# Kernel optimization log

Measured on AMD Instinct MI355X. Metric: run time of the kernel, lower is better.

The kernel has to match this reference:

```python
import jax, jax.numpy as jnp
import numpy as np
import math

IMG = 256      # image H = W (img_shape)
N_ANG = 360    # projection views over [0, pi)
N_DET = 256    # radial detector bins
N_SAMP = 256   # samples along each ray
VOX = 2.0      # voxel size / detector bin width in mm (isotropic)
FWHM = 4.0     # gaussian_PSF FWHM in mm


def _gauss_kernel(sigma):
    radius = max(1, int(math.ceil(3.0 * sigma)))
    t = np.arange(-radius, radius + 1, dtype=np.float64)
    k = np.exp(-0.5 * (t / sigma) ** 2)
    return (k / k.sum()).astype(np.float32), radius


def _blur_axis(x, sigma, axis):
    """1-D Gaussian blur with reflect padding along `axis` (static small kernel)."""
    k, r = _gauss_kernel(sigma)
    x = jnp.moveaxis(x, axis, -1)
    L = x.shape[-1]
    pad = [(0, 0)] * (x.ndim - 1) + [(r, r)]
    xp = jnp.pad(x, pad, mode='reflect')
    out = sum(float(k[i]) * xp[..., i:i + L] for i in range(2 * r + 1))
    return jnp.moveaxis(out, -1, axis)


def _blur2d(x, sigma):
    return _blur_axis(_blur_axis(x, sigma, -1), sigma, -2)


def _geometry():
    """Static parallel-beam ray-sampling geometry (bilinear taps, in pixel units)."""
    theta = np.pi * np.arange(N_ANG) / N_ANG
    r = (np.arange(N_DET) - (N_DET - 1) / 2.0) * VOX   # detector offsets [mm]
    s = (np.arange(N_SAMP) - (N_SAMP - 1) / 2.0) * VOX  # depth along ray [mm]
    cos = np.cos(theta)[:, None, None]
    sin = np.sin(theta)[:, None, None]
    x = r[None, :, None] * cos - s[None, None, :] * sin  # (A, D, S) mm
    y = r[None, :, None] * sin + s[None, None, :] * cos
    ix = x / VOX + (IMG - 1) / 2.0
    iy = y / VOX + (IMG - 1) / 2.0
    valid = ((ix >= 0) & (ix <= IMG - 1) & (iy >= 0) & (iy <= IMG - 1)).astype(np.float32)
    j0 = np.clip(np.floor(ix).astype(np.int32), 0, IMG - 2)
    i0 = np.clip(np.floor(iy).astype(np.int32), 0, IMG - 2)
    fx = (ix - j0).astype(np.float32)
    fy = (iy - i0).astype(np.float32)
    return i0, j0, fy, fx, valid

_GEO = tuple(jnp.asarray(a) for a in _geometry())


def _project(img):
    """Parallel-view 2D ray projection: img (B,H,W) -> sinogram (B, N_DET, N_ANG)."""
    i0, j0, fy, fx, valid = _GEO
    v00 = img[:, i0, j0]
    v01 = img[:, i0, j0 + 1]
    v10 = img[:, i0 + 1, j0]
    v11 = img[:, i0 + 1, j0 + 1]
    vals = ((1 - fy) * (1 - fx) * v00 + (1 - fy) * fx * v01
            + fy * (1 - fx) * v10 + fy * fx * v11) * valid
    sino = vals.sum(-1) * VOX          # (B, N_ANG, N_DET), line integral in mm
    return jnp.transpose(sino, (0, 2, 1))  # (B, N_DET, N_ANG)


def setup_inputs() -> dict:
    key = jax.random.key(0)
    k1, k2 = jax.random.split(key)
    image = jax.random.uniform(k1, (2, 1, IMG, IMG), dtype=jnp.float32)
    attenuation_map = jax.random.uniform(k2, (2, 1, IMG, IMG), dtype=jnp.float32)
    return {"image": image, "attenuation_map": attenuation_map}


def reference(image, attenuation_map):
    sqrt_log2 = math.sqrt(math.log(2.0))
    sigma_img = (FWHM / (4.0 * sqrt_log2)) / VOX
    # emission PSF blur (reflect) then project
    img_b = _blur2d(image, sigma_img)
    sino = _project(img_b[:, 0])[:, None]          # (B,1,N_DET,N_ANG)
    # attenuation: wider PSF blur, 0.01 scale, project, exponential scaling
    sigma_att = (FWHM / (2.0 * sqrt_log2)) / VOX
    att_b = _blur2d(attenuation_map, sigma_att) * 0.01
    att_sino = _project(att_b[:, 0])[:, None]
    sino = sino * jnp.exp(-att_sino * VOX)
    # column-wise (detector axis) sinogram PSF
    sino = _blur_axis(sino, sigma_img, -2)
    return sino
```

## Files before the change

kernel.cpp:

```cpp
#include <hip/hip_runtime.h>
#include <math.h>

#define IMG 256
#define N_ANG 360
#define N_DET 256

#define NH_BLOCKS 181
#define NV_BLOCKS (179 * 32)
#define EPS 1e-3f

struct W9 { float w[9]; };
struct AngTab { double c, sn; float cf, snf; float pad0, pad1; };

typedef _Float16 h2 __attribute__((ext_vector_type(2)));

#if __has_builtin(__builtin_amdgcn_fdot2)
__device__ __forceinline__ float fdot2(h2 a, h2 b, float c) {
    return __builtin_amdgcn_fdot2(a, b, c, false);
}
#else
__device__ __forceinline__ float fdot2(h2 a, h2 b, float c) {
    return c + (float)a[0] * (float)b[0] + (float)a[1] * (float)b[1];
}
#endif

__device__ __forceinline__ h2 as_h2(unsigned u) { return __builtin_bit_cast(h2, u); }
__device__ __forceinline__ unsigned pack2(float a, float b) {
    h2 v = { (_Float16)a, (_Float16)b };
    return __builtin_bit_cast(unsigned, v);
}

__device__ __forceinline__ int refl(int i, int L) {
    if (i < 0) i = -i;
    if (i >= L) i = 2 * (L - 1) - i;
    return i;
}

__global__ void blurpix_k(const float* __restrict__ img, const float* __restrict__ att,
                          uint4* __restrict__ pix2, AngTab* __restrict__ tab,
                          W9 wi, W9 wa) {
    int x = threadIdx.x, y = blockIdx.x;
    int gid = y * IMG + x;
    if (gid < N_ANG) {
        double th = M_PI * (double)gid / 360.0;
        double c = cos(th), sn = sin(th);
        AngTab tb;
        tb.c = c; tb.sn = sn; tb.cf = (float)c; tb.snf = (float)sn;
        tb.pad0 = 0.f; tb.pad1 = 0.f;
        tab[gid] = tb;
    }
    float v[4];
    #pragma unroll
    for (int m = 0; m < 4; ++m) {
        const float* src = ((m & 1) ? att : img) + (m >> 1) * IMG * IMG;
        const float* w = (m & 1) ? wa.w : wi.w;
        const int r = (m & 1) ? 4 : 2;
        float acc = 0.f;
        for (int dy = -r; dy <= r; ++dy) {
            const float* rowp = src + refl(y + dy, IMG) * IMG;
            float ra = 0.f;
            for (int dx = -r; dx <= r; ++dx) ra += w[dx + r] * rowp[refl(x + dx, IMG)];
            acc += w[dy + r] * ra;
        }
        v[m] = acc * ((m & 1) ? 0.01f : 1.0f);
    }
    __shared__ float4 row[IMG];
    row[x] = make_float4(v[0], v[1], v[2], v[3]);
    __syncthreads();
    float4 rn = row[min(x + 1, IMG - 1)];
    uint4 o;
    o.x = pack2(v[0], rn.x);
    o.y = pack2(v[1], rn.y);
    o.z = pack2(v[2], rn.z);
    o.w = pack2(v[3], rn.w);
    pix2[gid] = o;
}

template <typename P>
__device__ __forceinline__ int lastTrue(P p) {
    if (!p(0)) return -1;
    if (p(255)) return 255;
    int lo = 0, hi = 255;
    while (lo < hi) { int m = (lo + hi + 1) >> 1; if (p(m)) lo = m; else hi = m - 1; }
    return lo;
}
template <typename P>
__device__ __forceinline__ int firstTrue(P p) {
    if (!p(255)) return 256;
    if (p(0)) return 0;
    int lo = 0, hi = 255;
    while (lo < hi) { int m = (lo + hi) >> 1; if (p(m)) hi = m; else lo = m + 1; }
    return lo;
}

__device__ __forceinline__ void tap_acc(const uint4* __restrict__ pix2,
                                        int i0, int j0,
                                        float w00, float w01, float w10, float w11,
                                        float4& acc) {
    h2 wt = { (_Float16)w00, (_Float16)w01 };
    h2 wb = { (_Float16)w10, (_Float16)w11 };
    const uint4* p0 = pix2 + (i0 << 8) + j0;
    uint4 T = p0[0];
    uint4 B = p0[IMG];
    acc.x = fdot2(as_h2(T.x), wt, acc.x);
    acc.x = fdot2(as_h2(B.x), wb, acc.x);
    acc.y = fdot2(as_h2(T.y), wt, acc.y);
    acc.y = fdot2(as_h2(B.y), wb, acc.y);
    acc.z = fdot2(as_h2(T.z), wt, acc.z);
    acc.z = fdot2(as_h2(B.z), wb, acc.z);
    acc.w = fdot2(as_h2(T.w), wt, acc.w);
    acc.w = fdot2(as_h2(B.w), wb, acc.w);
}

__global__ __launch_bounds__(512) void proj_k(const uint4* __restrict__ pix2,
                                              const AngTab* __restrict__ tab,
                                              float4* __restrict__ part4,
                                              float* __restrict__ out, W9 wblur) {
    int t = threadIdx.x;
    int bx = blockIdx.x;

    if (bx < NH_BLOCKS) {
        int d = t & 255, kc = t >> 8;
        int a = (bx <= 90) ? bx : bx + 179;
        AngTab tb = tab[a];
        double rr = (double)(2 * d - 255);
        double rc = __dmul_rn(rr, tb.c), rs = __dmul_rn(rr, tb.sn);

        auto evIx = [&](int k) -> double {
            double ss = (double)(2 * k - 255);
            return __dadd_rn(__dmul_rn(__dsub_rn(rc, __dmul_rn(ss, tb.sn)), 0.5), 127.5);
        };
        auto evIy = [&](int k) -> double {
            double ss = (double)(2 * k - 255);
            return __dadd_rn(__dmul_rn(__dadd_rn(rs, __dmul_rn(ss, tb.c)), 0.5), 127.5);
        };
        int khiA = lastTrue([&](int k) { return evIx(k) >= 0.0; });
        int kloA = firstTrue([&](int k) { return evIx(k) <= 255.0; });
        int kloB, khiB;
        if (tb.c > 0.0) {
            kloB = firstTrue([&](int k) { return evIy(k) >= 0.0; });
            khiB = lastTrue([&](int k) { return evIy(k) <= 255.0; });
        } else {
            khiB = lastTrue([&](int k) { return evIy(k) >= 0.0; });
            kloB = firstTrue([&](int k) { return evIy(k) <= 255.0; });
        }
        int lo = max(kloA, kloB), hi = min(khiA, khiB);
        lo = max(lo, kc * 128); hi = min(hi, kc * 128 + 127);
        if (lo > hi) { lo = 0; hi = -1; }

        int jl = (hi >= lo) ? lo : 0x7fffffff;
        int jh = (hi >= lo) ? hi : (-0x7fffffff - 1);
        #pragma unroll
        for (int off = 32; off; off >>= 1) {
            jl = min(jl, __shfl_xor(jl, off));
            jh = max(jh, __shfl_xor(jh, off));
        }

        float x0f = (float)evIx(128);
        float y0f = (float)evIy(128);
        float dxf = -tb.snf, dyf = tb.cf;

        float4 acc = make_float4(0.f, 0.f, 0.f, 0.f);
        for (int kb = jl; kb <= jh; kb += 4) {
            #pragma unroll
            for (int u = 0; u < 4; ++u) {
                int k = kb + u;
                float kf = (float)(k - 128);
                float ixf = fmaf(kf, dxf, x0f);
                float iyf = fmaf(kf, dyf, y0f);
                float m = (k >= lo && k <= hi) ? 2.0f : 0.0f;
                int j0 = (int)ixf; j0 = min(max(j0, 0), 254);
                int i0 = (int)iyf; i0 = min(max(i0, 0), 254);
                float fx = ixf - (float)j0;
                float fy = iyf - (float)i0;
                float gxm = (1.f - fx) * m, fxm = fx * m;
                float gy = 1.f - fy;
                tap_acc(pix2, i0, j0, gy * gxm, gy * fxm, fy * gxm, fy * fxm, acc);
            }
        }

        __shared__ float4 red[512];
        __shared__ float vb[2][N_DET];
        red[t] = acc;
        __syncthreads();
        if (t < 256) {
            float4 u = red[t], v = red[t + 256];
            float si0 = u.x + v.x, sa0 = u.y + v.y;
            float si1 = u.z + v.z, sa1 = u.w + v.w;
            vb[0][t] = si0 * expf(-sa0 * 2.0f);
            vb[1][t] = si1 * expf(-sa1 * 2.0f);
        }
        __syncthreads();
        if (t < 256) {
            float a0 = 0.f, a1 = 0.f;
            #pragma unroll
            for (int i = -2; i <= 2; ++i) {
                int dd = refl(t + i, N_DET);
                a0 += wblur.w[i + 2] * vb[0][dd];
                a1 += wblur.w[i + 2] * vb[1][dd];
            }
            out[t * N_ANG + a] = a0;
            out[(N_DET + t) * N_ANG + a] = a1;
        }
    } else {
        int idx = bx - NH_BLOCKS;
        int a = 91 + (idx >> 5);
        int dgrp = idx & 31;
        int lane = t & 63, w = t >> 6;
        int d = dgrp * 8 + w;
        AngTab tb = tab[a];
        float cf = tb.cf, snf = tb.snf;
        float df = (float)d - 127.5f;
        float hx = fmaf(df, cf, 127.5f);
        float hy = fmaf(df, snf, 127.5f);

        float4 acc = make_float4(0.f, 0.f, 0.f, 0.f);
        #pragma unroll
        for (int j = 0; j < 4; ++j) {
            int k = j * 64 + lane;
            float kf = (float)k - 127.5f;
            float ixf = fmaf(-kf, snf, hx);
            float iyf = fmaf(kf, cf, hy);
            float vmin = fminf(fminf(ixf, 255.0f - ixf), fminf(iyf, 255.0f - iyf));
            if (!__any(vmin > -EPS)) continue;
            float m = (vmin >= EPS) ? 2.0f : 0.0f;
            if (fabsf(vmin) < EPS) {
                double ss = (double)(2 * k - 255);
                double rr = (double)(2 * d - 255);
                double rc = __dmul_rn(rr, tb.c), rs = __dmul_rn(rr, tb.sn);
                double ixd = __dadd_rn(__dmul_rn(__dsub_rn(rc, __dmul_rn(ss, tb.sn)), 0.5), 127.5);
                double iyd = __dadd_rn(__dmul_rn(__dadd_rn(rs, __dmul_rn(ss, tb.c)), 0.5), 127.5);
                bool v = (ixd >= 0.0) && (ixd <= 255.0) && (iyd >= 0.0) && (iyd <= 255.0);
                m = v ? 2.0f : 0.0f;
            }
            int j0 = (int)ixf; j0 = min(max(j0, 0), 254);
            int i0 = (int)iyf; i0 = min(max(i0, 0), 254);
            float fx = ixf - (float)j0;
            float fy = iyf - (float)i0;
            float gxm = (1.f - fx) * m, fxm = fx * m;
            float gy = 1.f - fy;
            tap_acc(pix2, i0, j0, gy * gxm, gy * fxm, fy * gxm, fy * fxm, acc);
        }

        #pragma unroll
        for (int off = 32; off; off >>= 1) {
            acc.x += __shfl_xor(acc.x, off);
            acc.y += __shfl_xor(acc.y, off);
            acc.z += __shfl_xor(acc.z, off);
            acc.w += __shfl_xor(acc.w, off);
        }
        if (lane == 0) part4[a * N_DET + d] = acc;
    }
}

__global__ __launch_bounds__(256) void finish_v_k(const float4* __restrict__ part4,
                                                  float* __restrict__ out, W9 wt) {
    int d = threadIdx.x;
    int b = blockIdx.x / 179;
    int a = 91 + (blockIdx.x % 179);
    float4 s = part4[a * N_DET + d];
    float si = b ? s.z : s.x;
    float sa = b ? s.w : s.y;
    __shared__ float vb[N_DET];
    vb[d] = si * expf(-sa * 2.0f);
    __syncthreads();
    float acc = 0.f;
    #pragma unroll
    for (int i = -2; i <= 2; ++i) acc += wt.w[i + 2] * vb[refl(d + i, N_DET)];
    out[(b * N_DET + d) * N_ANG + a] = acc;
}

static void gauss_w(W9* wt, double sigma, int r) {
    double tmp[9];
    double s = 0.0;
    for (int i = -r; i <= r; ++i) {
        double v = exp(-0.5 * ((double)i / sigma) * ((double)i / sigma));
        tmp[i + r] = v;
        s += v;
    }
    for (int i = 0; i < 9; ++i) wt->w[i] = 0.f;
    for (int i = 0; i < 2 * r + 1; ++i) wt->w[i] = (float)(tmp[i] / s);
}

extern "C" void kernel_launch(void* const* d_in, const int* in_sizes, int n_in,
                              void* d_out, int out_size, void* d_ws, size_t ws_size,
                              hipStream_t stream) {
    const float* img = (const float*)d_in[0];
    const float* att = (const float*)d_in[1];
    float* out = (float*)d_out;

    char* ws = (char*)d_ws;
    AngTab* tab = (AngTab*)ws;
    uint4* pix2 = (uint4*)(ws + 16384);
    float4* part4 = (float4*)(ws + 16384 + (1 << 20));

    double sqrt_log2 = sqrt(log(2.0));
    double sigma_img = 4.0 / (4.0 * sqrt_log2) / 2.0;
    double sigma_att = 4.0 / (2.0 * sqrt_log2) / 2.0;
    W9 wimg, watt;
    gauss_w(&wimg, sigma_img, 2);
    gauss_w(&watt, sigma_att, 4);

    blurpix_k<<<IMG, IMG, 0, stream>>>(img, att, pix2, tab, wimg, watt);
    proj_k<<<NH_BLOCKS + NV_BLOCKS, 512, 0, stream>>>(pix2, tab, part4, out, wimg);
    finish_v_k<<<2 * 179, N_DET, 0, stream>>>(part4, out, wimg);
}
```

Baseline: 58.07 us.

## Precompute ray intervals in blur kernel and split projection into finer blocks

```diff
diff --git a/kernel.cpp b/kernel.cpp
--- a/kernel.cpp
+++ b/kernel.cpp
@@ -5,8 +5,10 @@
 #define N_ANG 360
 #define N_DET 256
 
-#define NH_BLOCKS 181
-#define NV_BLOCKS (179 * 32)
+#define NHA 181
+#define KT 4
+#define NH_BLOCKS (NHA * KT)
+#define NV_BLOCKS (179 * 64)
 #define EPS 1e-3f
 
 struct W9 { float w[9]; };
@@ -36,8 +38,26 @@
     return i;
 }
 
+template <typename P>
+__device__ __forceinline__ int lastTrue(P p) {
+    if (!p(0)) return -1;
+    if (p(255)) return 255;
+    int lo = 0, hi = 255;
+    while (lo < hi) { int m = (lo + hi + 1) >> 1; if (p(m)) lo = m; else hi = m - 1; }
+    return lo;
+}
+template <typename P>
+__device__ __forceinline__ int firstTrue(P p) {
+    if (!p(255)) return 256;
+    if (p(0)) return 0;
+    int lo = 0, hi = 255;
+    while (lo < hi) { int m = (lo + hi) >> 1; if (p(m)) hi = m; else lo = m + 1; }
+    return lo;
+}
+
 __global__ void blurpix_k(const float* __restrict__ img, const float* __restrict__ att,
                           uint4* __restrict__ pix2, AngTab* __restrict__ tab,
+                          int2* __restrict__ ivl, float2* __restrict__ pos0,
                           W9 wi, W9 wa) {
     int x = threadIdx.x, y = blockIdx.x;
     int gid = y * IMG + x;
@@ -74,23 +94,36 @@
     o.z = pack2(v[2], rn.z);
     o.w = pack2(v[3], rn.w);
     pix2[gid] = o;
-}
-
-template <typename P>
-__device__ __forceinline__ int lastTrue(P p) {
-    if (!p(0)) return -1;
-    if (p(255)) return 255;
-    int lo = 0, hi = 255;
-    while (lo < hi) { int m = (lo + hi + 1) >> 1; if (p(m)) lo = m; else hi = m - 1; }
-    return lo;
-}
-template <typename P>
-__device__ __forceinline__ int firstTrue(P p) {
-    if (!p(255)) return 256;
-    if (p(0)) return 0;
-    int lo = 0, hi = 255;
-    while (lo < hi) { int m = (lo + hi) >> 1; if (p(m)) hi = m; else lo = m + 1; }
-    return lo;
+
+    if (y < NHA) {
+        int aidx = y, d = x;
+        int a = (aidx <= 90) ? aidx : aidx + 179;
+        double th = M_PI * (double)a / 360.0;
+        double c = cos(th), sn = sin(th);
+        double rr = (double)(2 * d - 255);
+        double rc = __dmul_rn(rr, c), rs = __dmul_rn(rr, sn);
+        auto evIx = [&](int k) -> double {
+            double ss = (double)(2 * k - 255);
+            return __dadd_rn(__dmul_rn(__dsub_rn(rc, __dmul_rn(ss, sn)), 0.5), 127.5);
+        };
+        auto evIy = [&](int k) -> double {
+            double ss = (double)(2 * k - 255);
+            return __dadd_rn(__dmul_rn(__dadd_rn(rs, __dmul_rn(ss, c)), 0.5), 127.5);
+        };
+        int khiA = lastTrue([&](int k) { return evIx(k) >= 0.0; });
+        int kloA = firstTrue([&](int k) { return evIx(k) <= 255.0; });
+        int kloB, khiB;
+        if (c > 0.0) {
+            kloB = firstTrue([&](int k) { return evIy(k) >= 0.0; });
+            khiB = lastTrue([&](int k) { return evIy(k) <= 255.0; });
+        } else {
+            khiB = lastTrue([&](int k) { return evIy(k) >= 0.0; });
+            kloB = firstTrue([&](int k) { return evIy(k) <= 255.0; });
+        }
+        int ray = aidx * N_DET + d;
+        ivl[ray] = make_int2(max(kloA, kloB), min(khiA, khiB));
+        pos0[ray] = make_float2((float)evIx(128), (float)evIy(128));
+    }
 }
 
 __device__ __forceinline__ void tap_acc(const uint4* __restrict__ pix2,
@@ -112,40 +145,25 @@
     acc.w = fdot2(as_h2(B.w), wb, acc.w);
 }
 
-__global__ __launch_bounds__(512) void proj_k(const uint4* __restrict__ pix2,
+__global__ __launch_bounds__(256) void proj_k(const uint4* __restrict__ pix2,
                                               const AngTab* __restrict__ tab,
-                                              float4* __restrict__ part4,
-                                              float* __restrict__ out, W9 wblur) {
+                                              const int2* __restrict__ ivl,
+                                              const float2* __restrict__ pos0,
+                                              float4* __restrict__ part4H,
+                                              float4* __restrict__ part4V) {
     int t = threadIdx.x;
     int bx = blockIdx.x;
 
     if (bx < NH_BLOCKS) {
-        int d = t & 255, kc = t >> 8;
-        int a = (bx <= 90) ? bx : bx + 179;
+        int aidx = bx >> 2, kt = bx & 3;
+        int d = t;
+        int a = (aidx <= 90) ? aidx : aidx + 179;
         AngTab tb = tab[a];
-        double rr = (double)(2 * d - 255);
-        double rc = __dmul_rn(rr, tb.c), rs = __dmul_rn(rr, tb.sn);
-
-        auto evIx = [&](int k) -> double {
-            double ss = (double)(2 * k - 255);
-            return __dadd_rn(__dmul_rn(__dsub_rn(rc, __dmul_rn(ss, tb.sn)), 0.5), 127.5);
-        };
-        auto evIy = [&](int k) -> double {
-            double ss = (double)(2 * k - 255);
-            return __dadd_rn(__dmul_rn(__dadd_rn(rs, __dmul_rn(ss, tb.c)), 0.5), 127.5);
-        };
-        int khiA = lastTrue([&](int k) { return evIx(k) >= 0.0; });
-        int kloA = firstTrue([&](int k) { return evIx(k) <= 255.0; });
-        int kloB, khiB;
-        if (tb.c > 0.0) {
-            kloB = firstTrue([&](int k) { return evIy(k) >= 0.0; });
-            khiB = lastTrue([&](int k) { return evIy(k) <= 255.0; });
-        } else {
-            khiB = lastTrue([&](int k) { return evIy(k) >= 0.0; });
-            kloB = firstTrue([&](int k) { return evIy(k) <= 255.0; });
-        }
-        int lo = max(kloA, kloB), hi = min(khiA, khiB);
-        lo = max(lo, kc * 128); hi = min(hi, kc * 128 + 127);
+        int ray = aidx * N_DET + d;
+        int2 iv = ivl[ray];
+        float2 p0 = pos0[ray];
+
+        int lo = max(iv.x, kt * 64), hi = min(iv.y, kt * 64 + 63);
         if (lo > hi) { lo = 0; hi = -1; }
 
         int jl = (hi >= lo) ? lo : 0x7fffffff;
@@ -156,8 +174,6 @@
             jh = max(jh, __shfl_xor(jh, off));
         }
 
-        float x0f = (float)evIx(128);
-        float y0f = (float)evIy(128);
         float dxf = -tb.snf, dyf = tb.cf;
 
         float4 acc = make_float4(0.f, 0.f, 0.f, 0.f);
@@ -166,8 +182,8 @@
             for (int u = 0; u < 4; ++u) {
                 int k = kb + u;
                 float kf = (float)(k - 128);
-                float ixf = fmaf(kf, dxf, x0f);
-                float iyf = fmaf(kf, dyf, y0f);
+                float ixf = fmaf(kf, dxf, p0.x);
+                float iyf = fmaf(kf, dyf, p0.y);
                 float m = (k >= lo && k <= hi) ? 2.0f : 0.0f;
                 int j0 = (int)ixf; j0 = min(max(j0, 0), 254);
                 int i0 = (int)iyf; i0 = min(max(i0, 0), 254);
@@ -178,36 +194,13 @@
                 tap_acc(pix2, i0, j0, gy * gxm, gy * fxm, fy * gxm, fy * fxm, acc);
             }
         }
-
-        __shared__ float4 red[512];
-        __shared__ float vb[2][N_DET];
-        red[t] = acc;
-        __syncthreads();
-        if (t < 256) {
-            float4 u = red[t], v = red[t + 256];
-            float si0 = u.x + v.x, sa0 = u.y + v.y;
-            float si1 = u.z + v.z, sa1 = u.w + v.w;
-            vb[0][t] = si0 * expf(-sa0 * 2.0f);
-            vb[1][t] = si1 * expf(-sa1 * 2.0f);
-        }
-        __syncthreads();
-        if (t < 256) {
-            float a0 = 0.f, a1 = 0.f;
-            #pragma unroll
-            for (int i = -2; i <= 2; ++i) {
-                int dd = refl(t + i, N_DET);
-                a0 += wblur.w[i + 2] * vb[0][dd];
-                a1 += wblur.w[i + 2] * vb[1][dd];
-            }
-            out[t * N_ANG + a] = a0;
-            out[(N_DET + t) * N_ANG + a] = a1;
-        }
+        part4H[(kt * NHA + aidx) * N_DET + d] = acc;
     } else {
         int idx = bx - NH_BLOCKS;
-        int a = 91 + (idx >> 5);
-        int dgrp = idx & 31;
+        int a = 91 + (idx >> 6);
+        int dgrp = idx & 63;
         int lane = t & 63, w = t >> 6;
-        int d = dgrp * 8 + w;
+        int d = dgrp * 4 + w;
         AngTab tb = tab[a];
         float cf = tb.cf, snf = tb.snf;
         float df = (float)d - 127.5f;
@@ -249,16 +242,28 @@
             acc.z += __shfl_xor(acc.z, off);
             acc.w += __shfl_xor(acc.w, off);
         }
-        if (lane == 0) part4[a * N_DET + d] = acc;
-    }
-}
-
-__global__ __launch_bounds__(256) void finish_v_k(const float4* __restrict__ part4,
-                                                  float* __restrict__ out, W9 wt) {
+        if (lane == 0) part4V[(a - 91) * N_DET + d] = acc;
+    }
+}
+
+__global__ __launch_bounds__(256) void finish_k(const float4* __restrict__ part4H,
+                                                const float4* __restrict__ part4V,
+                                                float* __restrict__ out, W9 wt) {
     int d = threadIdx.x;
-    int b = blockIdx.x / 179;
-    int a = 91 + (blockIdx.x % 179);
-    float4 s = part4[a * N_DET + d];
+    int b = blockIdx.x / N_ANG;
+    int a = blockIdx.x % N_ANG;
+    float4 s;
+    if (a <= 90 || a >= 270) {
+        int aidx = (a <= 90) ? a : a - 179;
+        s = make_float4(0.f, 0.f, 0.f, 0.f);
+        #pragma unroll
+        for (int kt = 0; kt < KT; ++kt) {
+            float4 q = part4H[(kt * NHA + aidx) * N_DET + d];
+            s.x += q.x; s.y += q.y; s.z += q.z; s.w += q.w;
+        }
+    } else {
+        s = part4V[(a - 91) * N_DET + d];
+    }
     float si = b ? s.z : s.x;
     float sa = b ? s.w : s.y;
     __shared__ float vb[N_DET];
@@ -290,9 +295,12 @@
     float* out = (float*)d_out;
 
     char* ws = (char*)d_ws;
-    AngTab* tab = (AngTab*)ws;
-    uint4* pix2 = (uint4*)(ws + 16384);
-    float4* part4 = (float4*)(ws + 16384 + (1 << 20));
+    AngTab* tab    = (AngTab*)ws;
+    uint4* pix2    = (uint4*)(ws + 16384);
+    int2* ivl      = (int2*)(ws + 16384 + (1 << 20));
+    float2* pos0   = (float2*)(ws + 16384 + (1 << 20) + (1 << 19));
+    float4* part4H = (float4*)(ws + 16384 + 2 * (1 << 20));
+    float4* part4V = (float4*)(ws + 16384 + 5 * (1 << 20));
 
     double sqrt_log2 = sqrt(log(2.0));
     double sigma_img = 4.0 / (4.0 * sqrt_log2) / 2.0;
@@ -301,7 +309,8 @@
     gauss_w(&wimg, sigma_img, 2);
     gauss_w(&watt, sigma_att, 4);
 
-    blurpix_k<<<IMG, IMG, 0, stream>>>(img, att, pix2, tab, wimg, watt);
-    proj_k<<<NH_BLOCKS + NV_BLOCKS, 512, 0, stream>>>(pix2, tab, part4, out, wimg);
-    finish_v_k<<<2 * 179, N_DET, 0, stream>>>(part4, out, wimg);
-}
+    blurpix_k<<<IMG, IMG, 0, stream>>>(img, att, pix2, tab, ivl, pos0, wimg, watt);
+    proj_k<<<NH_BLOCKS + NV_BLOCKS, 256, 0, stream>>>(pix2, tab, ivl, pos0,
+                                                      part4H, part4V);
+    finish_k<<<2 * N_ANG, N_DET, 0, stream>>>(part4H, part4V, out, wimg);
+}
```

New measurement: 59.93 us. +3.2%, slower.
